# Kernel tuning notes

Hardware: AMD Instinct MI355X
Metric: run time of the kernel (lower is better)

## Reference

```python
import jax, jax.numpy as jnp
import numpy as np

N_HEAD = 16
ROPE_BASE = 10000.0

def rotate_half(x):
    half = x.shape[-1] // 2
    return jnp.concatenate((-x[..., half:], x[..., :half]), axis=-1)

def rope_freqs(T, head_dim, dtype):
    inv_freq = 1.0 / (ROPE_BASE ** (jnp.arange(0, head_dim, 2, dtype=jnp.float32) / head_dim))
    t = jnp.arange(T, dtype=jnp.float32)
    freqs = t[:, None] * inv_freq[None, :]          # [T, head_dim//2]
    emb = jnp.concatenate((freqs, freqs), axis=-1)  # [T, head_dim]
    return emb.astype(dtype)

def setup_inputs() -> dict:
    key = jax.random.key(0)
    ks = jax.random.split(key, 9)
    B, T, C = 2, 2048, 1024
    s = 1.0 / np.sqrt(C)
    return {
        'x':  jax.random.normal(ks[0], (B, T, C), jnp.float32),
        'Wq': jax.random.normal(ks[1], (C, C), jnp.float32) * s,
        'bq': jnp.zeros((C,), jnp.float32),
        'Wk': jax.random.normal(ks[2], (C, C), jnp.float32) * s,
        'bk': jnp.zeros((C,), jnp.float32),
        'Wv': jax.random.normal(ks[3], (C, C), jnp.float32) * s,
        'bv': jnp.zeros((C,), jnp.float32),
        'Wp': jax.random.normal(ks[4], (C, C), jnp.float32) * s,
        'bp': jnp.zeros((C,), jnp.float32),
    }

def reference(x, Wq, bq, Wk, bk, Wv, bv, Wp, bp):
    B, T, C = x.shape
    H = N_HEAD
    D = C // H
    # torch Linear: y = x @ W.T + b
    def heads(y):
        return y.reshape(B, T, H, D).transpose(0, 2, 1, 3)  # [B,H,T,D]
    q = heads(x @ Wq.T + bq)
    k = heads(x @ Wk.T + bk)
    v = heads(x @ Wv.T + bv)
    # inline RoPE
    emb = rope_freqs(T, D, x.dtype)          # [T, D]
    cos, sin = jnp.cos(emb), jnp.sin(emb)
    q = q * cos + rotate_half(q) * sin
    k = k * cos + rotate_half(k) * sin
    # full T x T scores with causal masked softmax
    att = jnp.einsum('bhtd,bhsd->bhts', q, k) * (1.0 / jnp.sqrt(jnp.array(D, x.dtype)))
    causal = jnp.tril(jnp.ones((T, T), bool))
    att = jnp.where(causal[None, None], att, jnp.array(-jnp.inf, att.dtype))
    att = jax.nn.softmax(att, axis=-1)
    y = jnp.einsum('bhts,bhsd->bhtd', att, v)  # [B,H,T,D]
    y = y.transpose(0, 2, 1, 3).reshape(B, T, C)
    return y @ Wp.T + bp
```

## Files before the change

kernel.cpp:

```cpp
#include <hip/hip_runtime.h>
#include <hip/hip_bf16.h>
#include <stdint.h>

typedef unsigned short u16;
typedef __attribute__((ext_vector_type(8))) short bf16x8;
typedef __attribute__((ext_vector_type(4))) float f32x4;

typedef const __attribute__((address_space(1))) unsigned int* gu32p;
typedef __attribute__((address_space(3))) unsigned int* lu32p;

__device__ __forceinline__ void gl_lds16(const u16* g, u16* l) {
  __builtin_amdgcn_global_load_lds((gu32p)(const void*)g, (lu32p)(void*)l, 16, 0, 0);
}

__device__ __forceinline__ u16 f2bf(float f) {
  union { float f; unsigned u; } v; v.f = f;
  unsigned r = v.u + 0x7fffu + ((v.u >> 16) & 1u);
  return (u16)(r >> 16);
}
__device__ __forceinline__ void st2bf(u16* p0, u16* p1, float a, float b) {
  union { __hip_bfloat162 h; u16 u[2]; } cv;
  cv.h = __float22bfloat162_rn(make_float2(a, b));
  *p0 = cv.u[0]; *p1 = cv.u[1];
}

__global__ void convert_kernel(const float4* __restrict__ x, const float4* __restrict__ wq,
                               const float4* __restrict__ wk, const float4* __restrict__ wv,
                               const float4* __restrict__ wp,
                               u16* __restrict__ xb, u16* __restrict__ wqb, u16* __restrict__ wkb,
                               u16* __restrict__ wvb, u16* __restrict__ wpb,
                               float2* __restrict__ tab) {
  int i = blockIdx.x * 256 + threadIdx.x;
  const int NX = 1048576, NW = 262144, NCONV = NX + 4 * NW;
  if (i >= NCONV) {
    int j = i - NCONV;
    int d = j & 31, t = j >> 5;
    float ang = (float)t * expf(-0.28782313662425572f * (float)d);
    tab[j] = make_float2(cosf(ang), sinf(ang));
    return;
  }
  const float4* src; u16* dst; int off;
  if (i < NX)            { src = x;  dst = xb;  off = i; }
  else if (i < NX + NW)  { src = wq; dst = wqb; off = i - NX; }
  else if (i < NX + 2*NW){ src = wk; dst = wkb; off = i - NX - NW; }
  else if (i < NX + 3*NW){ src = wv; dst = wvb; off = i - NX - 2*NW; }
  else                   { src = wp; dst = wpb; off = i - NX - 3*NW; }
  float4 v = src[off];
  ushort4 ov = make_ushort4(f2bf(v.x), f2bf(v.y), f2bf(v.z), f2bf(v.w));
  *(ushort4*)&dst[off * 4] = ov;
}

template<int FUSE_ROPE, int OUT_BF16, int TRANS_V>
__global__ __launch_bounds__(256) void gemm_bt_kernel(
    const u16* __restrict__ A,
    const u16* __restrict__ B0, const u16* __restrict__ B1, const u16* __restrict__ B2,
    const float* __restrict__ bias0, const float* __restrict__ bias1, const float* __restrict__ bias2,
    void* out0, void* out1, void* out2, const float2* __restrict__ tab)
{
  __shared__ __align__(16) u16 As[2][4096];
  __shared__ __align__(16) u16 Bs[2][4096];
  const int z = blockIdx.z;
  const u16* Bw = (z == 0) ? B0 : (z == 1) ? B1 : B2;
  const float* bias = (z == 0) ? bias0 : (z == 1) ? bias1 : bias2;
  void* outv = (z == 0) ? out0 : (z == 1) ? out1 : out2;
  const int tid = threadIdx.x, lane = tid & 63, w = tid >> 6;
  const int wr = w >> 1, wc = w & 1;
  const int quad = lane >> 4, l15 = lane & 15;
  const int m0 = blockIdx.y * 128, n0 = blockIdx.x * 128;
  const int sr = lane >> 2, sc = (lane & 3) * 8;

  auto stg = [&](int kt, int bf) {
    const int k0 = kt * 32;
    #pragma unroll
    for (int p = 0; p < 2; p++) {
      gl_lds16(A  + (m0 + p*64 + w*16 + sr) * 1024 + k0 + sc, &As[bf][p*2048 + w*512]);
      gl_lds16(Bw + (n0 + p*64 + w*16 + sr) * 1024 + k0 + sc, &Bs[bf][p*2048 + w*512]);
    }
  };

  f32x4 acc[4][4] = {};
  stg(0, 0);
  for (int kt = 0; kt < 32; kt++) {
    __syncthreads();
    if (kt < 31) stg(kt + 1, (kt + 1) & 1);
    const int bf = kt & 1;
    bf16x8 af[4], bfr[4];
    #pragma unroll
    for (int mt = 0; mt < 4; mt++)
      af[mt] = *(const bf16x8*)&As[bf][(wr*64 + mt*16 + l15) * 32 + quad*8];
    #pragma unroll
    for (int nt = 0; nt < 4; nt++)
      bfr[nt] = *(const bf16x8*)&Bs[bf][(wc*64 + nt*16 + l15) * 32 + quad*8];
    #pragma unroll
    for (int mt = 0; mt < 4; mt++)
      #pragma unroll
      for (int nt = 0; nt < 4; nt++)
        acc[mt][nt] = __builtin_amdgcn_mfma_f32_16x16x32_bf16(af[mt], bfr[nt], acc[mt][nt], 0, 0, 0);
  }

  if (TRANS_V && z == 2) {
    const int bb = m0 >> 11, tg0 = (m0 & 2047) + wr*64 + quad*4;
    #pragma unroll
    for (int nt = 0; nt < 4; nt++) {
      const int c = n0 + wc*64 + nt*16 + l15;
      const float bv = bias[c];
      u16* vrow = (u16*)outv + (size_t)(bb*1024 + c) * 2048 + tg0;
      #pragma unroll
      for (int mt = 0; mt < 4; mt++) {
        ushort4 pk;
        pk.x = f2bf(acc[mt][nt][0] + bv); pk.y = f2bf(acc[mt][nt][1] + bv);
        pk.z = f2bf(acc[mt][nt][2] + bv); pk.w = f2bf(acc[mt][nt][3] + bv);
        *(ushort4*)&vrow[mt*16] = pk;
      }
    }
    return;
  }

  #pragma unroll
  for (int mt = 0; mt < 4; mt++) {
    #pragma unroll
    for (int r = 0; r < 4; r++) {
      const int row = m0 + wr*64 + mt*16 + quad*4 + r;
      float v[4];
      #pragma unroll
      for (int nt = 0; nt < 4; nt++)
        v[nt] = acc[mt][nt][r] + bias[n0 + wc*64 + nt*16 + l15];
      if (FUSE_ROPE && z < 2) {
        const int t = row & 2047;
        #pragma unroll
        for (int nt = 0; nt < 2; nt++) {
          const int d = nt*16 + l15;
          float2 cs = tab[t*32 + d];
          float x0 = v[nt], x1 = v[nt+2];
          v[nt]   = x0 * cs.x - x1 * cs.y;
          v[nt+2] = x1 * cs.x + x0 * cs.y;
        }
      }
      #pragma unroll
      for (int nt = 0; nt < 4; nt++) {
        const int col = n0 + wc*64 + nt*16 + l15;
        if (OUT_BF16) ((u16*)outv)[row * 1024 + col] = f2bf(v[nt]);
        else          ((float*)outv)[row * 1024 + col] = v[nt];
      }
    }
  }
}

__global__ __launch_bounds__(512) void attn_kernel(
    const u16* __restrict__ qg, const u16* __restrict__ kg,
    const u16* __restrict__ vtg, u16* __restrict__ yg)
{
  __shared__ __align__(16) u16 K_lds[2][128 * 64];
  __shared__ __align__(16) u16 V_lds[2][64 * 128];
  __shared__ __align__(16) u16 P_lds[8][2][16 * 128];
  const int x = blockIdx.x;
  const int hh = blockIdx.y, b = blockIdx.z;
  const int tid = threadIdx.x, lane = tid & 63, w = tid >> 6;
  const int wt = w >> 2;
  const int quad = lane >> 4, l15 = lane & 15;
  const int bh = b * (2048 * 1024) + hh * 64;
  const int vtb = (b * 16 + hh) * 131072;

  const int qtA = x, qtB = 15 - x;
  const int qt_w = wt ? qtB : qtA;
  const int wl = w & 3;

  bf16x8 qf[2][2];
  #pragma unroll
  for (int rg = 0; rg < 2; rg++) {
    const int qrow = qt_w*128 + rg*64 + wl*16 + l15;
    qf[rg][0] = *(const bf16x8*)&qg[bh + qrow*1024 + quad*8];
    qf[rg][1] = *(const bf16x8*)&qg[bh + qrow*1024 + 32 + quad*8];
  }
  f32x4 o[2][4] = {};
  f32x4 l5[2] = {};

  bf16x8 ones;
  #pragma unroll
  for (int i2 = 0; i2 < 8; i2++) ones[i2] = (short)0x3F80;

  const float c = 0.18033688011112042f;

  auto do_stage = [&](int j, int bf) {
    #pragma unroll
    for (int p = 0; p < 2; p++) {
      const int seg = w*2 + p;
      const int r = seg*8 + (lane >> 3);
      const int g = (lane & 7) ^ (r & 7);
      gl_lds16(kg + bh + (j*128 + r) * 1024 + g*8, &K_lds[bf][seg*512]);
    }
    #pragma unroll
    for (int p = 0; p < 2; p++) {
      const int seg = w*2 + p;
      const int r = seg*4 + (lane >> 4);
      const int g = (lane & 15) ^ (r & 15);
      gl_lds16(vtg + vtb + r * 2048 + j*128 + g*8, &V_lds[bf][seg*512]);
    }
  };

  do_stage(0, 0);
  for (int j = 0; j <= qtB; j++) {
    __syncthreads();
    if (j < qtB) do_stage(j + 1, (j + 1) & 1);
    const int bf = j & 1;
    if (wt == 0 && j > qtA) continue;
    const bool diag = (j == qt_w);

    f32x4 s[2][8];
    #pragma unroll
    for (int nt = 0; nt < 8; nt++) {
      const int krow = (nt*16 + l15) * 64;
      const int g0 = ((quad)     ^ (l15 & 7)) * 8;
      const int g1 = ((4 + quad) ^ (l15 & 7)) * 8;
      bf16x8 kf0 = *(const bf16x8*)&K_lds[bf][krow + g0];
      bf16x8 kf1 = *(const bf16x8*)&K_lds[bf][krow + g1];
      #pragma unroll
      for (int rg = 0; rg < 2; rg++) {
        f32x4 z = {};
        z = __builtin_amdgcn_mfma_f32_16x16x32_bf16(qf[rg][0], kf0, z, 0, 0, 0);
        z = __builtin_amdgcn_mfma_f32_16x16x32_bf16(qf[rg][1], kf1, z, 0, 0, 0);
        s[rg][nt] = z;
      }
    }
    if (diag) {
      #pragma unroll
      for (int rg = 0; rg < 2; rg++) {
        const int trow = rg*64 + wl*16 + quad*4;
        #pragma unroll
        for (int nt = 0; nt < 8; nt++)
          #pragma unroll
          for (int r = 0; r < 4; r++)
            if (nt*16 + l15 > trow + r) s[rg][nt][r] = -1e30f;
      }
    }
    #pragma unroll
    for (int rg = 0; rg < 2; rg++)
      #pragma unroll
      for (int r = 0; r < 4; r++) {
        const int R = quad*4 + r;
        u16* pp = &P_lds[w][rg][R*128 + (l15 & 7)];
        #pragma unroll
        for (int nt = 0; nt < 8; nt += 2) {
          float p0 = exp2f(s[rg][nt][r] * c);
          float p1 = exp2f(s[rg][nt+1][r] * c);
          const int g0 = ((nt*2     + (l15 >> 3)) ^ (R & 7)) * 8;
          const int g1 = (((nt+1)*2 + (l15 >> 3)) ^ (R & 7)) * 8;
          st2bf(pp + g0, pp + g1, p0, p1);
        }
      }
    #pragma unroll
    for (int ss = 0; ss < 4; ss++) {
      const int pg = ((ss*4 + quad) ^ (l15 & 7)) * 8;
      bf16x8 pf0 = *(const bf16x8*)&P_lds[w][0][l15*128 + pg];
      bf16x8 pf1 = *(const bf16x8*)&P_lds[w][1][l15*128 + pg];
      l5[0] = __builtin_amdgcn_mfma_f32_16x16x32_bf16(pf0, ones, l5[0], 0, 0, 0);
      l5[1] = __builtin_amdgcn_mfma_f32_16x16x32_bf16(pf1, ones, l5[1], 0, 0, 0);
      #pragma unroll
      for (int dt = 0; dt < 4; dt++) {
        const int vg = ((ss*4 + quad) ^ l15) * 8;
        bf16x8 vf = *(const bf16x8*)&V_lds[bf][(dt*16 + l15)*128 + vg];
        o[0][dt] = __builtin_amdgcn_mfma_f32_16x16x32_bf16(pf0, vf, o[0][dt], 0, 0, 0);
        o[1][dt] = __builtin_amdgcn_mfma_f32_16x16x32_bf16(pf1, vf, o[1][dt], 0, 0, 0);
      }
    }
  }

  #pragma unroll
  for (int rg = 0; rg < 2; rg++)
    #pragma unroll
    for (int r = 0; r < 4; r++) {
      float inv = 1.0f / l5[rg][r];
      u16* yr = &yg[bh + (qt_w*128 + rg*64 + wl*16 + quad*4 + r) * 1024 + l15];
      st2bf(yr,      yr + 16, o[rg][0][r] * inv, o[rg][1][r] * inv);
      st2bf(yr + 32, yr + 48, o[rg][2][r] * inv, o[rg][3][r] * inv);
    }
}

extern "C" void kernel_launch(void* const* d_in, const int* in_sizes, int n_in,
                              void* d_out, int out_size, void* d_ws, size_t ws_size,
                              hipStream_t stream) {
  const float* x  = (const float*)d_in[0];
  const float* Wq = (const float*)d_in[1];
  const float* bq = (const float*)d_in[2];
  const float* Wk = (const float*)d_in[3];
  const float* bk = (const float*)d_in[4];
  const float* Wv = (const float*)d_in[5];
  const float* bv = (const float*)d_in[6];
  const float* Wp = (const float*)d_in[7];
  const float* bp = (const float*)d_in[8];

  char* ws = (char*)d_ws;
  u16* xb  = (u16*)(ws);
  u16* wqb = (u16*)(ws + (8u  << 20));
  u16* wkb = (u16*)(ws + (10u << 20));
  u16* wvb = (u16*)(ws + (12u << 20));
  u16* wpb = (u16*)(ws + (14u << 20));
  u16* qb  = (u16*)(ws + (16u << 20));
  u16* kb  = (u16*)(ws + (24u << 20));
  u16* vtb = (u16*)(ws + (32u << 20));
  float2* tab = (float2*)(ws + (40u << 20));
  u16* yb = xb;

  convert_kernel<<<8448, 256, 0, stream>>>((const float4*)x, (const float4*)Wq, (const float4*)Wk,
                                           (const float4*)Wv, (const float4*)Wp,
                                           xb, wqb, wkb, wvb, wpb, tab);
  gemm_bt_kernel<1, 1, 1><<<dim3(8, 32, 3), 256, 0, stream>>>(xb, wqb, wkb, wvb, bq, bk, bv,
                                                              (void*)qb, (void*)kb, (void*)vtb, tab);
  attn_kernel<<<dim3(8, 16, 2), 512, 0, stream>>>(qb, kb, vtb, yb);
  gemm_bt_kernel<0, 0, 0><<<dim3(8, 32, 1), 256, 0, stream>>>(yb, wpb, wpb, wpb, bp, bp, bp,
                                                              (void*)d_out, (void*)d_out, (void*)d_out, tab);
}
```

Before: 210.1 us.

## Keep softmax probabilities in registers via transposed QK MFMA and permlane swaps

The score MFMA operands are swapped so S^T is produced, and the exponentiated probabilities are packed to bf16 and rearranged across lanes with permlane32/permlane16 swaps into the A-operand layout for the PV MFMA. This removes the per-wave P_lds shared-memory buffer and its store/load round trip, and interleaves score computation with PV accumulation per 32-column slice. It cuts LDS traffic and LDS footprint, which may raise occupancy, at the cost of extra cross-lane permute instructions and reliance on gfx950-specific builtins.

Measured after the change: 210.7 us. Within noise of the previous version (+0.3%).

```diff
diff --git a/kernel.cpp b/kernel.cpp
--- a/kernel.cpp
+++ b/kernel.cpp
@@ -5,6 +5,7 @@
 typedef unsigned short u16;
 typedef __attribute__((ext_vector_type(8))) short bf16x8;
 typedef __attribute__((ext_vector_type(4))) float f32x4;
+typedef __attribute__((ext_vector_type(2))) unsigned int u32x2;
 
 typedef const __attribute__((address_space(1))) unsigned int* gu32p;
 typedef __attribute__((address_space(3))) unsigned int* lu32p;
@@ -22,6 +23,11 @@
   union { __hip_bfloat162 h; u16 u[2]; } cv;
   cv.h = __float22bfloat162_rn(make_float2(a, b));
   *p0 = cv.u[0]; *p1 = cv.u[1];
+}
+__device__ __forceinline__ unsigned pk2bf(float a, float b) {
+  union { __hip_bfloat162 h; unsigned u; } cv;
+  cv.h = __float22bfloat162_rn(make_float2(a, b));
+  return cv.u;
 }
 
 __global__ void convert_kernel(const float4* __restrict__ x, const float4* __restrict__ wq,
@@ -152,7 +158,6 @@
 {
   __shared__ __align__(16) u16 K_lds[2][128 * 64];
   __shared__ __align__(16) u16 V_lds[2][64 * 128];
-  __shared__ __align__(16) u16 P_lds[8][2][16 * 128];
   const int x = blockIdx.x;
   const int hh = blockIdx.y, b = blockIdx.z;
   const int tid = threadIdx.x, lane = tid & 63, w = tid >> 6;
@@ -206,61 +211,61 @@
     if (wt == 0 && j > qtA) continue;
     const bool diag = (j == qt_w);
 
-    f32x4 s[2][8];
-    #pragma unroll
-    for (int nt = 0; nt < 8; nt++) {
-      const int krow = (nt*16 + l15) * 64;
-      const int g0 = ((quad)     ^ (l15 & 7)) * 8;
-      const int g1 = ((4 + quad) ^ (l15 & 7)) * 8;
-      bf16x8 kf0 = *(const bf16x8*)&K_lds[bf][krow + g0];
-      bf16x8 kf1 = *(const bf16x8*)&K_lds[bf][krow + g1];
+    #pragma unroll
+    for (int ss = 0; ss < 4; ss++) {
+      f32x4 s[2][2];
+      #pragma unroll
+      for (int h = 0; h < 2; h++) {
+        const int nt = ss*2 + h;
+        const int krow = (nt*16 + l15) * 64;
+        const int g0 = ((quad)     ^ (l15 & 7)) * 8;
+        const int g1 = ((4 + quad) ^ (l15 & 7)) * 8;
+        bf16x8 kf0 = *(const bf16x8*)&K_lds[bf][krow + g0];
+        bf16x8 kf1 = *(const bf16x8*)&K_lds[bf][krow + g1];
+        #pragma unroll
+        for (int rg = 0; rg < 2; rg++) {
+          f32x4 z = {};
+          z = __builtin_amdgcn_mfma_f32_16x16x32_bf16(kf0, qf[rg][0], z, 0, 0, 0);
+          z = __builtin_amdgcn_mfma_f32_16x16x32_bf16(kf1, qf[rg][1], z, 0, 0, 0);
+          s[rg][h] = z;
+        }
+      }
+      if (diag) {
+        #pragma unroll
+        for (int rg = 0; rg < 2; rg++) {
+          const int qrow = rg*64 + wl*16 + l15;
+          #pragma unroll
+          for (int h = 0; h < 2; h++)
+            #pragma unroll
+            for (int r = 0; r < 4; r++)
+              if ((ss*2 + h)*16 + quad*4 + r > qrow) s[rg][h][r] = -1e30f;
+        }
+      }
+      bf16x8 pa[2];
       #pragma unroll
       for (int rg = 0; rg < 2; rg++) {
-        f32x4 z = {};
-        z = __builtin_amdgcn_mfma_f32_16x16x32_bf16(qf[rg][0], kf0, z, 0, 0, 0);
-        z = __builtin_amdgcn_mfma_f32_16x16x32_bf16(qf[rg][1], kf1, z, 0, 0, 0);
-        s[rg][nt] = z;
-      }
-    }
-    if (diag) {
-      #pragma unroll
-      for (int rg = 0; rg < 2; rg++) {
-        const int trow = rg*64 + wl*16 + quad*4;
-        #pragma unroll
-        for (int nt = 0; nt < 8; nt++)
-          #pragma unroll
-          for (int r = 0; r < 4; r++)
-            if (nt*16 + l15 > trow + r) s[rg][nt][r] = -1e30f;
-      }
-    }
-    #pragma unroll
-    for (int rg = 0; rg < 2; rg++)
-      #pragma unroll
-      for (int r = 0; r < 4; r++) {
-        const int R = quad*4 + r;
-        u16* pp = &P_lds[w][rg][R*128 + (l15 & 7)];
-        #pragma unroll
-        for (int nt = 0; nt < 8; nt += 2) {
-          float p0 = exp2f(s[rg][nt][r] * c);
-          float p1 = exp2f(s[rg][nt+1][r] * c);
-          const int g0 = ((nt*2     + (l15 >> 3)) ^ (R & 7)) * 8;
-          const int g1 = (((nt+1)*2 + (l15 >> 3)) ^ (R & 7)) * 8;
-          st2bf(pp + g0, pp + g1, p0, p1);
-        }
-      }
-    #pragma unroll
-    for (int ss = 0; ss < 4; ss++) {
-      const int pg = ((ss*4 + quad) ^ (l15 & 7)) * 8;
-      bf16x8 pf0 = *(const bf16x8*)&P_lds[w][0][l15*128 + pg];
-      bf16x8 pf1 = *(const bf16x8*)&P_lds[w][1][l15*128 + pg];
-      l5[0] = __builtin_amdgcn_mfma_f32_16x16x32_bf16(pf0, ones, l5[0], 0, 0, 0);
-      l5[1] = __builtin_amdgcn_mfma_f32_16x16x32_bf16(pf1, ones, l5[1], 0, 0, 0);
+        float a0 = exp2f(s[rg][0][0] * c), a1 = exp2f(s[rg][0][1] * c);
+        float a2 = exp2f(s[rg][0][2] * c), a3 = exp2f(s[rg][0][3] * c);
+        float b0 = exp2f(s[rg][1][0] * c), b1 = exp2f(s[rg][1][1] * c);
+        float b2 = exp2f(s[rg][1][2] * c), b3 = exp2f(s[rg][1][3] * c);
+        unsigned A01 = pk2bf(a0, a1), A23 = pk2bf(a2, a3);
+        unsigned B01 = pk2bf(b0, b1), B23 = pk2bf(b2, b3);
+        u32x2 t0 = __builtin_amdgcn_permlane32_swap(A01, B01, false, false);
+        u32x2 w02 = __builtin_amdgcn_permlane16_swap(t0[0], t0[1], false, false);
+        u32x2 t1 = __builtin_amdgcn_permlane32_swap(A23, B23, false, false);
+        u32x2 w13 = __builtin_amdgcn_permlane16_swap(t1[0], t1[1], false, false);
+        union { unsigned u[4]; bf16x8 v; } pk;
+        pk.u[0] = w02[0]; pk.u[1] = w13[0]; pk.u[2] = w02[1]; pk.u[3] = w13[1];
+        pa[rg] = pk.v;
+      }
+      l5[0] = __builtin_amdgcn_mfma_f32_16x16x32_bf16(pa[0], ones, l5[0], 0, 0, 0);
+      l5[1] = __builtin_amdgcn_mfma_f32_16x16x32_bf16(pa[1], ones, l5[1], 0, 0, 0);
       #pragma unroll
       for (int dt = 0; dt < 4; dt++) {
         const int vg = ((ss*4 + quad) ^ l15) * 8;
         bf16x8 vf = *(const bf16x8*)&V_lds[bf][(dt*16 + l15)*128 + vg];
-        o[0][dt] = __builtin_amdgcn_mfma_f32_16x16x32_bf16(pf0, vf, o[0][dt], 0, 0, 0);
-        o[1][dt] = __builtin_amdgcn_mfma_f32_16x16x32_bf16(pf1, vf, o[1][dt], 0, 0, 0);
+        o[0][dt] = __builtin_amdgcn_mfma_f32_16x16x32_bf16(pa[0], vf, o[0][dt], 0, 0, 0);
+        o[1][dt] = __builtin_amdgcn_mfma_f32_16x16x32_bf16(pa[1], vf, o[1][dt], 0, 0, 0);
       }
     }
   }
```
